# Optimization experiments

Hardware: AMD Instinct MI355X
Metric: run time of the kernel (lower is better)

Reference implementation:

```python
import math
import jax, jax.numpy as jnp
import numpy as np

QDEPTH = 8
WIDTH = 32
HEIGHT = 32
PIXELS = WIDTH * HEIGHT          # 1024
WIRES = int(math.ceil(math.log2(PIXELS)))  # 10, and PIXELS == 2**WIRES exactly
BATCH = 2048


def setup_inputs() -> dict:
    key = jax.random.key(0)
    k1, k2 = jax.random.split(key)
    x = jax.random.normal(k1, (BATCH, 1, WIDTH, HEIGHT), dtype=jnp.float32)
    # torch.randn(weight_shape) * 0.4
    weights = jax.random.normal(k2, (QDEPTH, WIRES, 3), dtype=jnp.float32) * 0.4
    return {"x": x, "weights": weights, "reps": 1}


def _apply_1q(s, U, wire):
    # s: (batch, 2, 2, ..., 2); apply 2x2 unitary U on qubit `wire` (axis wire+1)
    ax = wire + 1
    s = jnp.moveaxis(s, ax, -1)
    s = s @ U.T                      # new[..., i] = sum_j U[i, j] * old[..., j]
    return jnp.moveaxis(s, -1, ax)


def _apply_cnot(s, ctrl, tgt):
    # flip target bit on the control==1 half of the state
    c_ax = ctrl + 1
    t_ax = tgt + 1
    s0 = jnp.take(s, 0, axis=c_ax)
    s1 = jnp.take(s, 1, axis=c_ax)
    t = t_ax - 1 if t_ax > c_ax else t_ax
    s1 = jnp.flip(s1, axis=t)
    return jnp.stack([s0, s1], axis=c_ax)


def _rot_matrix(phi, theta, omega):
    # qml.Rot = RZ(phi) -> RY(theta) -> RZ(omega)
    c = jnp.cos(theta * 0.5)
    sn = jnp.sin(theta * 0.5)
    ep = jnp.exp(-0.5j * (phi + omega))   # e^{-i(phi+omega)/2}
    em = jnp.exp(-0.5j * (phi - omega))   # e^{-i(phi-omega)/2}
    return jnp.stack([
        jnp.stack([ep * c, -jnp.conj(em) * sn]),
        jnp.stack([em * sn, jnp.conj(ep) * c]),
    ]).astype(jnp.complex64)


def _circuit(psi, weights, reps):
    # psi: (batch, 2**WIRES) complex64 normalized state
    b = psi.shape[0]
    s = psi.reshape((b,) + (2,) * WIRES)
    w = jnp.tanh(weights)                 # qw_map.tanh
    # StronglyEntanglingLayers default ranges: r_l = l % (wires-1) + 1
    ranges = [(l % (WIRES - 1)) + 1 for l in range(QDEPTH)]
    for _ in range(reps):
        for l in range(QDEPTH):
            for q in range(WIRES):
                U = _rot_matrix(w[l, q, 0], w[l, q, 1], w[l, q, 2])
                s = _apply_1q(s, U, q)
            r = ranges[l]
            for q in range(WIRES):
                s = _apply_cnot(s, q, (q + r) % WIRES)
    return s.reshape(b, 2 ** WIRES)


def reference(x, weights, reps):
    b = x.shape[0]
    v = x.reshape(b, PIXELS)                       # b 1 w h -> b (w h)
    old_norm = jnp.linalg.norm(v, axis=-1, keepdims=True)
    psi = (v / old_norm).astype(jnp.complex64)     # real amplitudes, zero imag
    out = _circuit(psi, weights, reps)
    out = out * old_norm.astype(jnp.complex64)
    return out.reshape(b, 1, WIDTH, HEIGHT)
```

## Files before the change

### kernel.cpp

```cpp
#include <hip/hip_runtime.h>
#include <math.h>


#define WIRES   10
#define NSTATE  1024
#define QDEPTH  8
#define NBATCH  2048
#define NGATES  (QDEPTH * WIRES)

typedef float v2f __attribute__((ext_vector_type(2)));
typedef unsigned int v2u __attribute__((ext_vector_type(2)));
static __device__ __forceinline__ v2f s2(float x) { return (v2f){x, x}; }

__device__ __forceinline__ int perm_g(int j, int r) {
#pragma unroll
    for (int q = WIRES - 1; q >= 0; --q) {
        const int cb = 9 - q;
        const int tb = 9 - ((q + r) % WIRES);
        j ^= ((j >> cb) & 1) << tb;
    }
    return j;
}

template<int CTRL>
__device__ __forceinline__ float dppmov(float x) {
    return __int_as_float(__builtin_amdgcn_update_dpp(
        0, __float_as_int(x), CTRL, 0xF, 0xF, true));
}
#define FX1(v)  dppmov<0xB1>(v)
#define FX2(v)  dppmov<0x4E>(v)
#define FX4(v)  dppmov<0x1B>(dppmov<0x141>(v))
#define FX8(v)  dppmov<0x128>(v)

#if __has_builtin(__builtin_amdgcn_permlane16_swap)
static __device__ __forceinline__ float pl16swap(float x) {
    const v2u r = __builtin_amdgcn_permlane16_swap(
        __float_as_uint(x), __float_as_uint(x), false, false);
    return __uint_as_float((threadIdx.x & 16) ? r.x : r.y);
}
#define FX16(v) pl16swap(v)
#else
#define FX16(v) __shfl_xor((v), 16, 64)
#endif

#if __has_builtin(__builtin_amdgcn_permlane32_swap)
static __device__ __forceinline__ float pl32swap(float x) {
    const v2u r = __builtin_amdgcn_permlane32_swap(
        __float_as_uint(x), __float_as_uint(x), false, false);
    return __uint_as_float((threadIdx.x & 32) ? r.x : r.y);
}
#define FX32(v) pl32swap(v)
#else
#define FX32(v) __shfl_xor((v), 32, 64)
#endif

#define APPLY_LOCAL_PK(uptr, mask)                                            \
    {                                                                         \
        const float* __restrict__ u = (uptr);                                 \
        const float u00r=u[0], u00i=u[1], u01r=u[2], u01i=u[3];               \
        const float u10r=u[4], u10i=u[5], u11r=u[6], u11i=u[7];               \
        _Pragma("unroll")                                                     \
        for (int k0 = 0; k0 < 8; ++k0) {                                      \
            if (k0 & (mask)) continue;                                        \
            const int k1 = k0 | (mask);                                       \
            const v2f a0r = zr[k0], a0i = zi[k0];                             \
            const v2f a1r = zr[k1], a1i = zi[k1];                             \
            zr[k0] = s2(u00r)*a0r - s2(u00i)*a0i + s2(u01r)*a1r - s2(u01i)*a1i;\
            zi[k0] = s2(u00r)*a0i + s2(u00i)*a0r + s2(u01r)*a1i + s2(u01i)*a1r;\
            zr[k1] = s2(u10r)*a0r - s2(u10i)*a0i + s2(u11r)*a1r - s2(u11i)*a1i;\
            zi[k1] = s2(u10r)*a0i + s2(u10i)*a0r + s2(u11r)*a1i + s2(u11i)*a1r;\
        }                                                                     \
    }

#define LANE_GATE_PK(W, J, FETCH)                                             \
    {                                                                         \
        const float* __restrict__ u = gw + (W) * 8;                           \
        const bool hi = (lane >> (J)) & 1;                                    \
        const float c0r = hi ? u[6] : u[0], c0i = hi ? u[7] : u[1];           \
        const float c1r = hi ? u[4] : u[2], c1i = hi ? u[5] : u[3];           \
        _Pragma("unroll")                                                     \
        for (int k = 0; k < 8; ++k) {                                         \
            v2f pr, pi;                                                       \
            pr.x = FETCH(zr[k].x); pr.y = FETCH(zr[k].y);                     \
            pi.x = FETCH(zi[k].x); pi.y = FETCH(zi[k].y);                     \
            const v2f sr = zr[k], si = zi[k];                                 \
            zr[k] = s2(c0r)*sr - s2(c0i)*si + s2(c1r)*pr - s2(c1i)*pi;        \
            zi[k] = s2(c0r)*si + s2(c0i)*sr + s2(c1r)*pi + s2(c1i)*pr;        \
        }                                                                     \
    }

__global__ __launch_bounds__(64) void qsim_fused(
    const float* __restrict__ x,
    const float* __restrict__ weights,
    float* __restrict__ out,
    const int interleaved)
{
    __shared__ float lds[2 * NSTATE];
    __shared__ float cf[NGATES * 8];
    __shared__ int   gtl[QDEPTH * 16];
    __shared__ int   gaT[QDEPTH * 64];

    const int lane = threadIdx.x;
    const int b    = blockIdx.x;

    for (int g = lane; g < NGATES; g += 64) {
        const float phi   = tanhf(weights[g * 3 + 0]);
        const float theta = tanhf(weights[g * 3 + 1]);
        const float omega = tanhf(weights[g * 3 + 2]);
        const float c  = cosf(theta * 0.5f);
        const float sn = sinf(theta * 0.5f);
        const float a  = 0.5f * (phi + omega);
        const float bb = 0.5f * (phi - omega);
        const float ca = cosf(a),  sa = sinf(a);
        const float cb = cosf(bb), sb = sinf(bb);
        cf[g * 8 + 0] =  ca * c;  cf[g * 8 + 1] = -sa * c;
        cf[g * 8 + 2] = -cb * sn; cf[g * 8 + 3] = -sb * sn;
        cf[g * 8 + 4] =  cb * sn; cf[g * 8 + 5] = -sb * sn;
        cf[g * 8 + 6] =  ca * c;  cf[g * 8 + 7] =  sa * c;
    }
    for (int e = lane; e < QDEPTH * 16; e += 64) {
        const int l = e >> 4, t = e & 15;
        const int j = perm_g(t, l + 1);
        gtl[e] = ((j & 15) << 6) | (j >> 4);
    }
#pragma unroll
    for (int l = 0; l < QDEPTH; ++l) {
        const int j = perm_g(lane << 4, l + 1);
        gaT[l * 64 + lane] = ((j & 15) << 6) | (j >> 4);
    }

    v2f zr[8], zi[8];

    const float4* __restrict__ x4 =
        (const float4*)(x + ((size_t)b << 10) + (lane << 4));
    {
        const float4 v0 = x4[0], v1 = x4[1], v2 = x4[2], v3 = x4[3];
        zr[0].x=v0.x; zr[1].x=v0.y; zr[2].x=v0.z; zr[3].x=v0.w;
        zr[4].x=v1.x; zr[5].x=v1.y; zr[6].x=v1.z; zr[7].x=v1.w;
        zr[0].y=v2.x; zr[1].y=v2.y; zr[2].y=v2.z; zr[3].y=v2.w;
        zr[4].y=v3.x; zr[5].y=v3.y; zr[6].y=v3.z; zr[7].y=v3.w;
#pragma unroll
        for (int k = 0; k < 8; ++k) zi[k] = (v2f){0.f, 0.f};
    }

    for (int l = 0; l < QDEPTH; ++l) {
        const float* __restrict__ gw = cf + l * 80;

        APPLY_LOCAL_PK(gw + 9*8, 1)
        APPLY_LOCAL_PK(gw + 8*8, 2)
        APPLY_LOCAL_PK(gw + 7*8, 4)

        {
            const float* __restrict__ u = gw + 6*8;
            const v2f pAr = (v2f){u[0], u[6]};
            const v2f pAi = (v2f){u[1], u[7]};
            const v2f pBr = (v2f){u[2], u[4]};
            const v2f pBi = (v2f){u[3], u[5]};
#pragma unroll
            for (int k = 0; k < 8; ++k) {
                const v2f r  = zr[k], i = zi[k];
                const v2f rs = __builtin_shufflevector(r, r, 1, 0);
                const v2f is = __builtin_shufflevector(i, i, 1, 0);
                zr[k] = pAr*r - pAi*i + pBr*rs - pBi*is;
                zi[k] = pAr*i + pAi*r + pBr*is + pBi*rs;
            }
        }

        LANE_GATE_PK(5, 0, FX1)
        LANE_GATE_PK(4, 1, FX2)
        LANE_GATE_PK(3, 2, FX4)
        LANE_GATE_PK(2, 3, FX8)
        LANE_GATE_PK(1, 4, FX16)
        LANE_GATE_PK(0, 5, FX32)

#pragma unroll
        for (int k = 0; k < 8; ++k) {
            const int w = k * 64 + lane;
            lds[w]        = zr[k].x;
            lds[w + 512]  = zr[k].y;
            lds[w + 1024] = zi[k].x;
            lds[w + 1536] = zi[k].y;
        }
        const int ga = gaT[l * 64 + lane];
#pragma unroll
        for (int k = 0; k < 8; ++k) {
            const int a0 = ga ^ gtl[l * 16 + k];
            const int a1 = ga ^ gtl[l * 16 + k + 8];
            zr[k].x = lds[a0]; zi[k].x = lds[a0 + 1024];
            zr[k].y = lds[a1]; zi[k].y = lds[a1 + 1024];
        }
    }

    if (interleaved) {
        float2* __restrict__ o2 = (float2*)out;
        const size_t base = ((size_t)b << 10) + (lane << 4);
#pragma unroll
        for (int k = 0; k < 8; ++k) {
            o2[base + k]     = make_float2(zr[k].x, zi[k].x);
            o2[base + k + 8] = make_float2(zr[k].y, zi[k].y);
        }
    } else {
        float4* __restrict__ o4 = (float4*)(out + ((size_t)b << 10) + (lane << 4));
        o4[0] = make_float4(zr[0].x, zr[1].x, zr[2].x, zr[3].x);
        o4[1] = make_float4(zr[4].x, zr[5].x, zr[6].x, zr[7].x);
        o4[2] = make_float4(zr[0].y, zr[1].y, zr[2].y, zr[3].y);
        o4[3] = make_float4(zr[4].y, zr[5].y, zr[6].y, zr[7].y);
    }
}

extern "C" void kernel_launch(void* const* d_in, const int* in_sizes, int n_in,
                              void* d_out, int out_size, void* d_ws, size_t ws_size,
                              hipStream_t stream) {
    const float* x       = (const float*)d_in[0];
    const float* weights = (const float*)d_in[1];
    float* out = (float*)d_out;
    const int interleaved = (out_size >= 2 * NBATCH * NSTATE) ? 1 : 0;
    (void)d_ws; (void)ws_size;

    qsim_fused<<<NBATCH, 64, 0, stream>>>(x, weights, out, interleaved);
}
```

Measured before the change: 102.3 us.

## Keep gate coefficients in registers and broadcast them with readlane instead of LDS

Each lane now computes the coefficients of one or two gates into registers. Every gate's coefficients are fetched as wave-uniform scalars through readlane, so the per-gate LDS table reads are gone. The permutation XOR offsets are rebuilt from four readlane'd basis values per layer rather than loaded from a 16-entry LDS table. Together these aim to cut LDS traffic and latency inside the layer loop, at the cost of many readlane instructions (VALU to SGPR moves) and more register pressure from the coefficient arrays.

```diff
diff --git a/kernel.cpp b/kernel.cpp
--- a/kernel.cpp
+++ b/kernel.cpp
@@ -22,6 +22,19 @@
     return j;
 }
 
+#if __has_builtin(__builtin_amdgcn_readlane)
+static __device__ __forceinline__ int rli(int v, int idx) {
+    return __builtin_amdgcn_readlane(v, idx);
+}
+#else
+static __device__ __forceinline__ int rli(int v, int idx) {
+    return __shfl(v, idx, 64);
+}
+#endif
+static __device__ __forceinline__ float rlf(float v, int idx) {
+    return __int_as_float(rli(__float_as_int(v), idx));
+}
+
 template<int CTRL>
 __device__ __forceinline__ float dppmov(float x) {
     return __int_as_float(__builtin_amdgcn_update_dpp(
@@ -54,15 +67,33 @@
 #define FX32(v) __shfl_xor((v), 32, 64)
 #endif
 
-#define APPLY_LOCAL_PK(uptr, mask)                                            \
+__device__ __forceinline__ void gate_coeffs(
+    const float* __restrict__ w, int g, float (&c8)[8])
+{
+    const float phi   = tanhf(w[g * 3 + 0]);
+    const float theta = tanhf(w[g * 3 + 1]);
+    const float omega = tanhf(w[g * 3 + 2]);
+    const float c  = cosf(theta * 0.5f);
+    const float sn = sinf(theta * 0.5f);
+    const float a  = 0.5f * (phi + omega);
+    const float bb = 0.5f * (phi - omega);
+    const float ca = cosf(a),  sa = sinf(a);
+    const float cb = cosf(bb), sb = sinf(bb);
+    c8[0] =  ca * c;  c8[1] = -sa * c;
+    c8[2] = -cb * sn; c8[3] = -sb * sn;
+    c8[4] =  cb * sn; c8[5] = -sb * sn;
+    c8[6] =  ca * c;  c8[7] =  sa * c;
+}
+
+#define LOCAL_GATE(Q, MASK)                                                   \
     {                                                                         \
-        const float* __restrict__ u = (uptr);                                 \
-        const float u00r=u[0], u00i=u[1], u01r=u[2], u01i=u[3];               \
-        const float u10r=u[4], u10i=u[5], u11r=u[6], u11i=u[7];               \
+        const float u00r=getc(Q,0), u00i=getc(Q,1), u01r=getc(Q,2),           \
+                    u01i=getc(Q,3), u10r=getc(Q,4), u10i=getc(Q,5),           \
+                    u11r=getc(Q,6), u11i=getc(Q,7);                           \
         _Pragma("unroll")                                                     \
         for (int k0 = 0; k0 < 8; ++k0) {                                      \
-            if (k0 & (mask)) continue;                                        \
-            const int k1 = k0 | (mask);                                       \
+            if (k0 & (MASK)) continue;                                        \
+            const int k1 = k0 | (MASK);                                       \
             const v2f a0r = zr[k0], a0i = zi[k0];                             \
             const v2f a1r = zr[k1], a1i = zi[k1];                             \
             zr[k0] = s2(u00r)*a0r - s2(u00i)*a0i + s2(u01r)*a1r - s2(u01i)*a1i;\
@@ -72,12 +103,33 @@
         }                                                                     \
     }
 
-#define LANE_GATE_PK(W, J, FETCH)                                             \
+#define HSWAP_GATE(Q)                                                         \
     {                                                                         \
-        const float* __restrict__ u = gw + (W) * 8;                           \
+        const float u00r=getc(Q,0), u00i=getc(Q,1), u01r=getc(Q,2),           \
+                    u01i=getc(Q,3), u10r=getc(Q,4), u10i=getc(Q,5),           \
+                    u11r=getc(Q,6), u11i=getc(Q,7);                           \
+        const v2f pAr = (v2f){u00r, u11r};                                    \
+        const v2f pAi = (v2f){u00i, u11i};                                    \
+        const v2f pBr = (v2f){u01r, u10r};                                    \
+        const v2f pBi = (v2f){u01i, u10i};                                    \
+        _Pragma("unroll")                                                     \
+        for (int k = 0; k < 8; ++k) {                                         \
+            const v2f r  = zr[k], i = zi[k];                                  \
+            const v2f rs = __builtin_shufflevector(r, r, 1, 0);               \
+            const v2f is = __builtin_shufflevector(i, i, 1, 0);               \
+            zr[k] = pAr*r - pAi*i + pBr*rs - pBi*is;                          \
+            zi[k] = pAr*i + pAi*r + pBr*is + pBi*rs;                          \
+        }                                                                     \
+    }
+
+#define LANE_GATE(Q, J, FETCH)                                                \
+    {                                                                         \
+        const float u00r=getc(Q,0), u00i=getc(Q,1), u01r=getc(Q,2),           \
+                    u01i=getc(Q,3), u10r=getc(Q,4), u10i=getc(Q,5),           \
+                    u11r=getc(Q,6), u11i=getc(Q,7);                           \
         const bool hi = (lane >> (J)) & 1;                                    \
-        const float c0r = hi ? u[6] : u[0], c0i = hi ? u[7] : u[1];           \
-        const float c1r = hi ? u[4] : u[2], c1i = hi ? u[5] : u[3];           \
+        const float c0r = hi ? u11r : u00r, c0i = hi ? u11i : u00i;           \
+        const float c1r = hi ? u10r : u01r, c1i = hi ? u10i : u01i;           \
         _Pragma("unroll")                                                     \
         for (int k = 0; k < 8; ++k) {                                         \
             v2f pr, pi;                                                       \
@@ -89,39 +141,64 @@
         }                                                                     \
     }
 
-__global__ __launch_bounds__(64) void qsim_fused(
+template<typename GetC>
+__device__ __forceinline__ void layer_body(
+    v2f (&zr)[8], v2f (&zi)[8], GetC getc,
+    const int G0, const int G1, const int G2, const int G3,
+    const int ga, float* __restrict__ lds, const int lane)
+{
+    LOCAL_GATE(9, 1)
+    LOCAL_GATE(8, 2)
+    LOCAL_GATE(7, 4)
+    HSWAP_GATE(6)
+    LANE_GATE(5, 0, FX1)
+    LANE_GATE(4, 1, FX2)
+    LANE_GATE(3, 2, FX4)
+    LANE_GATE(2, 3, FX8)
+    LANE_GATE(1, 4, FX16)
+    LANE_GATE(0, 5, FX32)
+
+#pragma unroll
+    for (int k = 0; k < 8; ++k) {
+        const int w = k * 64 + lane;
+        lds[w]        = zr[k].x;
+        lds[w + 512]  = zr[k].y;
+        lds[w + 1024] = zi[k].x;
+        lds[w + 1536] = zi[k].y;
+    }
+    const int s01 = G0 ^ G1;
+    const int gkt[8] = {0, G0, G1, s01, G2, G2 ^ G0, G2 ^ G1, G2 ^ s01};
+#pragma unroll
+    for (int k = 0; k < 8; ++k) {
+        const int a0 = ga ^ gkt[k];
+        const int a1 = a0 ^ G3;
+        zr[k].x = lds[a0]; zi[k].x = lds[a0 + 1024];
+        zr[k].y = lds[a1]; zi[k].y = lds[a1 + 1024];
+    }
+}
+
+__global__ __launch_bounds__(64) void qsim_rl(
     const float* __restrict__ x,
     const float* __restrict__ weights,
     float* __restrict__ out,
     const int interleaved)
 {
     __shared__ float lds[2 * NSTATE];
-    __shared__ float cf[NGATES * 8];
-    __shared__ int   gtl[QDEPTH * 16];
     __shared__ int   gaT[QDEPTH * 64];
 
     const int lane = threadIdx.x;
     const int b    = blockIdx.x;
 
-    for (int g = lane; g < NGATES; g += 64) {
-        const float phi   = tanhf(weights[g * 3 + 0]);
-        const float theta = tanhf(weights[g * 3 + 1]);
-        const float omega = tanhf(weights[g * 3 + 2]);
-        const float c  = cosf(theta * 0.5f);
-        const float sn = sinf(theta * 0.5f);
-        const float a  = 0.5f * (phi + omega);
-        const float bb = 0.5f * (phi - omega);
-        const float ca = cosf(a),  sa = sinf(a);
-        const float cb = cosf(bb), sb = sinf(bb);
-        cf[g * 8 + 0] =  ca * c;  cf[g * 8 + 1] = -sa * c;
-        cf[g * 8 + 2] = -cb * sn; cf[g * 8 + 3] = -sb * sn;
-        cf[g * 8 + 4] =  cb * sn; cf[g * 8 + 5] = -sb * sn;
-        cf[g * 8 + 6] =  ca * c;  cf[g * 8 + 7] =  sa * c;
-    }
-    for (int e = lane; e < QDEPTH * 16; e += 64) {
-        const int l = e >> 4, t = e & 15;
-        const int j = perm_g(t, l + 1);
-        gtl[e] = ((j & 15) << 6) | (j >> 4);
+    float cA[8], cB[8];
+    gate_coeffs(weights, lane, cA);
+    gate_coeffs(weights, 64 + (lane & 15), cB);
+
+    int gv;
+    {
+        const int lg = (lane >> 2) & 7;
+        const int bb = lane & 3;
+        const int j  = perm_g(1 << bb, lg + 1);
+        gv = ((j & 15) << 6) | (j >> 4);
     }
 #pragma unroll
     for (int l = 0; l < QDEPTH; ++l) {
@@ -130,7 +207,6 @@
     }
 
     v2f zr[8], zi[8];
-
     const float4* __restrict__ x4 =
         (const float4*)(x + ((size_t)b << 10) + (lane << 4));
     {
@@ -143,52 +219,38 @@
         for (int k = 0; k < 8; ++k) zi[k] = (v2f){0.f, 0.f};
     }
 
-    for (int l = 0; l < QDEPTH; ++l) {
-        const float* __restrict__ gw = cf + l * 80;
-
-        APPLY_LOCAL_PK(gw + 9*8, 1)
-        APPLY_LOCAL_PK(gw + 8*8, 2)
-        APPLY_LOCAL_PK(gw + 7*8, 4)
-
-        {
-            const float* __restrict__ u = gw + 6*8;
-            const v2f pAr = (v2f){u[0], u[6]};
-            const v2f pAi = (v2f){u[1], u[7]};
-            const v2f pBr = (v2f){u[2], u[4]};
-            const v2f pBi = (v2f){u[3], u[5]};
-#pragma unroll
-            for (int k = 0; k < 8; ++k) {
-                const v2f r  = zr[k], i = zi[k];
-                const v2f rs = __builtin_shufflevector(r, r, 1, 0);
-                const v2f is = __builtin_shufflevector(i, i, 1, 0);
-                zr[k] = pAr*r - pAi*i + pBr*rs - pBi*is;
-                zi[k] = pAr*i + pAi*r + pBr*is + pBi*rs;
-            }
-        }
-
-        LANE_GATE_PK(5, 0, FX1)
-        LANE_GATE_PK(4, 1, FX2)
-        LANE_GATE_PK(3, 2, FX4)
-        LANE_GATE_PK(2, 3, FX8)
-        LANE_GATE_PK(1, 4, FX16)
-        LANE_GATE_PK(0, 5, FX32)
-
-#pragma unroll
-        for (int k = 0; k < 8; ++k) {
-            const int w = k * 64 + lane;
-            lds[w]        = zr[k].x;
-            lds[w + 512]  = zr[k].y;
-            lds[w + 1024] = zi[k].x;
-            lds[w + 1536] = zi[k].y;
-        }
-        const int ga = gaT[l * 64 + lane];
-#pragma unroll
-        for (int k = 0; k < 8; ++k) {
-            const int a0 = ga ^ gtl[l * 16 + k];
-            const int a1 = ga ^ gtl[l * 16 + k + 8];
-            zr[k].x = lds[a0]; zi[k].x = lds[a0 + 1024];
-            zr[k].y = lds[a1]; zi[k].y = lds[a1 + 1024];
-        }
+    int ga = gaT[lane];
+
+#pragma unroll 1
+    for (int l = 0; l < 6; ++l) {
+        const int sb = l * 10;
+        const int G0 = rli(gv, 4 * l + 0);
+        const int G1 = rli(gv, 4 * l + 1);
+        const int G2 = rli(gv, 4 * l + 2);
+        const int G3 = rli(gv, 4 * l + 3);
+        const int ga_nx = gaT[(l + 1) * 64 + lane];
+        layer_body(zr, zi,
+            [&](int q, int j) { return rlf(cA[j], sb + q); },
+            G0, G1, G2, G3, ga, lds, lane);
+        ga = ga_nx;
+    }
+    {
+        const int G0 = rli(gv, 24), G1 = rli(gv, 25);
+        const int G2 = rli(gv, 26), G3 = rli(gv, 27);
+        const int ga_nx = gaT[7 * 64 + lane];
+        layer_body(zr, zi,
+            [&](int q, int j) {
+                return (q < 4) ? rlf(cA[j], 60 + q) : rlf(cB[j], q - 4);
+            },
+            G0, G1, G2, G3, ga, lds, lane);
+        ga = ga_nx;
+    }
+    {
+        const int G0 = rli(gv, 28), G1 = rli(gv, 29);
+        const int G2 = rli(gv, 30), G3 = rli(gv, 31);
+        layer_body(zr, zi,
+            [&](int q, int j) { return rlf(cB[j], 6 + q); },
+            G0, G1, G2, G3, ga, lds, lane);
     }
 
     if (interleaved) {
@@ -217,5 +279,5 @@
     const int interleaved = (out_size >= 2 * NBATCH * NSTATE) ? 1 : 0;
     (void)d_ws; (void)ws_size;
 
-    qsim_fused<<<NBATCH, 64, 0, stream>>>(x, weights, out, interleaved);
-}
+    qsim_rl<<<NBATCH, 64, 0, stream>>>(x, weights, out, interleaved);
+}
```

Result: slower. 108.2 us (+5.7%).

## Track CNOT layers as lazy GF(2) basis changes instead of per-layer LDS permutes

Applied to the files above, without the earlier changes.

Replaces the per-layer LDS scatter/gather that implemented each CNOT ring with a compile-time GF(2) linear map tracking, so each rotation gate acts on a transformed bit mask with sign parity corrections, and only one final LDS permutation is done. Gate coefficients are computed in registers per lane and broadcast via readlane rather than staged through shared memory tables. This removes 7 LDS round trips and the shared-memory tables, at the cost of gates whose masks span multiple bits needing compound cross-lane xor shuffles and extra parity selects.

```diff
diff --git a/kernel.cpp b/kernel.cpp
--- a/kernel.cpp
+++ b/kernel.cpp
@@ -12,8 +12,7 @@
 typedef unsigned int v2u __attribute__((ext_vector_type(2)));
 static __device__ __forceinline__ v2f s2(float x) { return (v2f){x, x}; }
 
-__device__ __forceinline__ int perm_g(int j, int r) {
-#pragma unroll
+constexpr int perm_gc(int j, int r) {
     for (int q = WIRES - 1; q >= 0; --q) {
         const int cb = 9 - q;
         const int tb = 9 - ((q + r) % WIRES);
@@ -22,15 +21,65 @@
     return j;
 }
 
+struct QTab {
+    int m[QDEPTH][10];
+    int hi[QDEPTH][10];
+    int fin[10];
+};
+
+constexpr QTab build_qtab() {
+    QTab T{};
+    int m[10], fr[10];
+    for (int b = 0; b < 10; ++b) { m[b] = 1 << b; fr[b] = 1 << b; }
+    for (int l = 0; l < QDEPTH; ++l) {
+        for (int b = 0; b < 10; ++b) { T.m[l][b] = m[b]; T.hi[l][b] = fr[b]; }
+        const int r = (l % (WIRES - 1)) + 1;
+        int nm[10], nf[10];
+        for (int b = 0; b < 10; ++b) {
+            const int u = perm_gc(1 << b, r);
+            int acc = 0;
+            for (int c = 0; c < 10; ++c) if ((u >> c) & 1) acc ^= m[c];
+            nm[b] = acc;
+        }
+        int gi[10];
+        for (int b = 0; b < 10; ++b) gi[b] = 1 << b;
+        for (int q = 0; q <= 9; ++q) {
+            const int cb = 9 - q;
+            const int tb = 9 - ((q + r) % WIRES);
+            gi[tb] ^= gi[cb];
+        }
+        for (int b = 0; b < 10; ++b) {
+            int acc = 0;
+            for (int c = 0; c < 10; ++c) if ((gi[b] >> c) & 1) acc ^= fr[c];
+            nf[b] = acc;
+        }
+        for (int b = 0; b < 10; ++b) { m[b] = nm[b]; fr[b] = nf[b]; }
+    }
+    for (int b = 0; b < 10; ++b) T.fin[b] = m[b];
+    return T;
+}
+
+constexpr QTab QT = build_qtab();
+constexpr int word_map(int x) { return ((x & 15) << 6) | (x >> 4); }
+
+#if __has_builtin(__builtin_amdgcn_readlane)
+static __device__ __forceinline__ int rli(int v, int idx) {
+    return __builtin_amdgcn_readlane(v, idx);
+}
+#else
+static __device__ __forceinline__ int rli(int v, int idx) {
+    return __shfl(v, idx, 64);
+}
+#endif
+static __device__ __forceinline__ float rlf(float v, int idx) {
+    return __int_as_float(rli(__float_as_int(v), idx));
+}
+
 template<int CTRL>
 __device__ __forceinline__ float dppmov(float x) {
     return __int_as_float(__builtin_amdgcn_update_dpp(
         0, __float_as_int(x), CTRL, 0xF, 0xF, true));
 }
-#define FX1(v)  dppmov<0xB1>(v)
-#define FX2(v)  dppmov<0x4E>(v)
-#define FX4(v)  dppmov<0x1B>(dppmov<0x141>(v))
-#define FX8(v)  dppmov<0x128>(v)
 
 #if __has_builtin(__builtin_amdgcn_permlane16_swap)
 static __device__ __forceinline__ float pl16swap(float x) {
@@ -38,9 +87,10 @@
         __float_as_uint(x), __float_as_uint(x), false, false);
     return __uint_as_float((threadIdx.x & 16) ? r.x : r.y);
 }
-#define FX16(v) pl16swap(v)
 #else
-#define FX16(v) __shfl_xor((v), 16, 64)
+static __device__ __forceinline__ float pl16swap(float x) {
+    return __shfl_xor(x, 16, 64);
+}
 #endif
 
 #if __has_builtin(__builtin_amdgcn_permlane32_swap)
@@ -49,88 +99,144 @@
         __float_as_uint(x), __float_as_uint(x), false, false);
     return __uint_as_float((threadIdx.x & 32) ? r.x : r.y);
 }
-#define FX32(v) pl32swap(v)
 #else
-#define FX32(v) __shfl_xor((v), 32, 64)
+static __device__ __forceinline__ float pl32swap(float x) {
+    return __shfl_xor(x, 32, 64);
+}
 #endif
 
-#define APPLY_LOCAL_PK(uptr, mask)                                            \
+template<int ML>
+__device__ __forceinline__ float fxor(float x) {
+    float v = x;
+    constexpr int low = ML & 15;
+    if constexpr (low >= 4 && low <= 7)  v = dppmov<0x141>(v);
+    if constexpr (low >= 8 && low <= 11) v = dppmov<0x128>(v);
+    if constexpr (low >= 12)             v = dppmov<0x140>(v);
+    constexpr int q = (low < 4) ? low
+                    : (low < 8) ? (low ^ 7)
+                    : (low < 12) ? (low ^ 8) : (low ^ 15);
+    if constexpr (q == 1) v = dppmov<0xB1>(v);
+    if constexpr (q == 2) v = dppmov<0x4E>(v);
+    if constexpr (q == 3) v = dppmov<0x1B>(v);
+    if constexpr (ML & 16) v = pl16swap(v);
+    if constexpr (ML & 32) v = pl32swap(v);
+    return v;
+}
+
+template<int MH, int ML>
+__device__ __forceinline__ v2f fetch_pair(v2f v) {
+    v2f s;
+    if constexpr (MH) s = __builtin_shufflevector(v, v, 1, 0);
+    else              s = v;
+    if constexpr (ML != 0) { s.x = fxor<ML>(s.x); s.y = fxor<ML>(s.y); }
+    return s;
+}
+
+__device__ __forceinline__ void gate_coeffs4(
+    const float* __restrict__ w, int g, float (&c4)[4])
+{
+    const float phi   = tanhf(w[g * 3 + 0]);
+    const float theta = tanhf(w[g * 3 + 1]);
+    const float omega = tanhf(w[g * 3 + 2]);
+    const float c  = cosf(theta * 0.5f);
+    const float sn = sinf(theta * 0.5f);
+    const float a  = 0.5f * (phi + omega);
+    const float bb = 0.5f * (phi - omega);
+    const float ca = cosf(a),  sa = sinf(a);
+    const float cb = cosf(bb), sb = sinf(bb);
+    c4[0] =  ca * c;
+    c4[1] = -sa * c;
+    c4[2] = -cb * sn;
+    c4[3] = -sb * sn;
+}
+
+template<int M, int HI>
+__device__ __forceinline__ void gate_apply(
+    v2f (&zr)[8], v2f (&zi)[8],
+    const float u00r, const float u00i,
+    const float u01r, const float u01i, const int lane)
+{
+    constexpr int mk = M & 7;
+    constexpr int mh = (M >> 3) & 1;
+    constexpr int ml = M >> 4;
+    constexpr int hk = HI & 7;
+    constexpr int hh = (HI >> 3) & 1;
+    constexpr int hl = HI >> 4;
+
+    unsigned sL = 0u;
+    if constexpr (hl != 0)
+        sL = ((unsigned)(__popc(lane & hl) & 1)) << 31;
+
+    const float b0  = __uint_as_float(__float_as_uint(u00i) ^ sL);
+    const float b0n = __uint_as_float(__float_as_uint(b0) ^ 0x80000000u);
+    const float r0  = __uint_as_float(__float_as_uint(u01r) ^ sL);
+    const float r0n = __uint_as_float(__float_as_uint(r0) ^ 0x80000000u);
+    const v2f C0i0 = (v2f){b0,  hh ? b0n : b0};
+    const v2f C0i1 = (v2f){b0n, hh ? b0  : b0n};
+    const v2f C1r0 = (v2f){r0,  hh ? r0n : r0};
+    const v2f C1r1 = (v2f){r0n, hh ? r0  : r0n};
+    const v2f C0r  = s2(u00r);
+    const v2f C1i  = s2(u01i);
+
+#define QG_MATH(KK, PR, PI)                                                   \
     {                                                                         \
-        const float* __restrict__ u = (uptr);                                 \
-        const float u00r=u[0], u00i=u[1], u01r=u[2], u01i=u[3];               \
-        const float u10r=u[4], u10i=u[5], u11r=u[6], u11i=u[7];               \
-        _Pragma("unroll")                                                     \
-        for (int k0 = 0; k0 < 8; ++k0) {                                      \
-            if (k0 & (mask)) continue;                                        \
-            const int k1 = k0 | (mask);                                       \
-            const v2f a0r = zr[k0], a0i = zi[k0];                             \
-            const v2f a1r = zr[k1], a1i = zi[k1];                             \
-            zr[k0] = s2(u00r)*a0r - s2(u00i)*a0i + s2(u01r)*a1r - s2(u01i)*a1i;\
-            zi[k0] = s2(u00r)*a0i + s2(u00i)*a0r + s2(u01r)*a1i + s2(u01i)*a1r;\
-            zr[k1] = s2(u10r)*a0r - s2(u10i)*a0i + s2(u11r)*a1r - s2(u11i)*a1i;\
-            zi[k1] = s2(u10r)*a0i + s2(u10i)*a0r + s2(u11r)*a1i + s2(u11i)*a1r;\
-        }                                                                     \
-    }
-
-#define LANE_GATE_PK(W, J, FETCH)                                             \
-    {                                                                         \
-        const float* __restrict__ u = gw + (W) * 8;                           \
-        const bool hi = (lane >> (J)) & 1;                                    \
-        const float c0r = hi ? u[6] : u[0], c0i = hi ? u[7] : u[1];           \
-        const float c1r = hi ? u[4] : u[2], c1i = hi ? u[5] : u[3];           \
-        _Pragma("unroll")                                                     \
-        for (int k = 0; k < 8; ++k) {                                         \
-            v2f pr, pi;                                                       \
-            pr.x = FETCH(zr[k].x); pr.y = FETCH(zr[k].y);                     \
-            pi.x = FETCH(zi[k].x); pi.y = FETCH(zi[k].y);                     \
-            const v2f sr = zr[k], si = zi[k];                                 \
-            zr[k] = s2(c0r)*sr - s2(c0i)*si + s2(c1r)*pr - s2(c1i)*pi;        \
-            zi[k] = s2(c0r)*si + s2(c0i)*sr + s2(c1r)*pi + s2(c1i)*pr;        \
-        }                                                                     \
-    }
-
-__global__ __launch_bounds__(64) void qsim_fused(
+        const bool pc1 = (__popc((KK) & hk) & 1) != 0;                        \
+        const v2f C0i = pc1 ? C0i1 : C0i0;                                    \
+        const v2f C1r = pc1 ? C1r1 : C1r0;                                    \
+        const v2f sr = zr[(KK)], si = zi[(KK)];                               \
+        zr[(KK)] = C0r*sr - C0i*si + C1r*(PR) - C1i*(PI);                     \
+        zi[(KK)] = C0r*si + C0i*sr + C1r*(PI) + C1i*(PR);                     \
+    }
+
+    if constexpr (mk == 0) {
+#pragma unroll
+        for (int k = 0; k < 8; ++k) {
+            const v2f pr = fetch_pair<mh, ml>(zr[k]);
+            const v2f pi = fetch_pair<mh, ml>(zi[k]);
+            QG_MATH(k, pr, pi)
+        }
+    } else {
+#pragma unroll
+        for (int k0 = 0; k0 < 8; ++k0) {
+            if ((k0 ^ mk) < k0) continue;
+            const int k1 = k0 ^ mk;
+            const v2f p0r = fetch_pair<mh, ml>(zr[k1]);
+            const v2f p0i = fetch_pair<mh, ml>(zi[k1]);
+            const v2f p1r = fetch_pair<mh, ml>(zr[k0]);
+            const v2f p1i = fetch_pair<mh, ml>(zi[k0]);
+            QG_MATH(k0, p0r, p0i)
+            QG_MATH(k1, p1r, p1i)
+        }
+    }
+#undef QG_MATH
+}
+
+#define GA(L, B, G) gate_apply<QT.m[L][B], QT.hi[L][B]>(zr, zi,               \
+    rlf(cA[0], G), rlf(cA[1], G), rlf(cA[2], G), rlf(cA[3], G), lane);
+#define GB(L, B, G) gate_apply<QT.m[L][B], QT.hi[L][B]>(zr, zi,               \
+    rlf(cB[0], G), rlf(cB[1], G), rlf(cB[2], G), rlf(cB[3], G), lane);
+
+#define LAYER_A(L)                                                            \
+    GA(L, 0, (L)*10 + 9) GA(L, 1, (L)*10 + 8) GA(L, 2, (L)*10 + 7)            \
+    GA(L, 3, (L)*10 + 6) GA(L, 4, (L)*10 + 5) GA(L, 5, (L)*10 + 4)            \
+    GA(L, 6, (L)*10 + 3) GA(L, 7, (L)*10 + 2) GA(L, 8, (L)*10 + 1)            \
+    GA(L, 9, (L)*10 + 0)
+
+__global__ __launch_bounds__(64) void qsim_lazy(
     const float* __restrict__ x,
     const float* __restrict__ weights,
     float* __restrict__ out,
     const int interleaved)
 {
     __shared__ float lds[2 * NSTATE];
-    __shared__ float cf[NGATES * 8];
-    __shared__ int   gtl[QDEPTH * 16];
-    __shared__ int   gaT[QDEPTH * 64];
-
     const int lane = threadIdx.x;
     const int b    = blockIdx.x;
 
-    for (int g = lane; g < NGATES; g += 64) {
-        const float phi   = tanhf(weights[g * 3 + 0]);
-        const float theta = tanhf(weights[g * 3 + 1]);
-        const float omega = tanhf(weights[g * 3 + 2]);
-        const float c  = cosf(theta * 0.5f);
-        const float sn = sinf(theta * 0.5f);
-        const float a  = 0.5f * (phi + omega);
-        const float bb = 0.5f * (phi - omega);
-        const float ca = cosf(a),  sa = sinf(a);
-        const float cb = cosf(bb), sb = sinf(bb);
-        cf[g * 8 + 0] =  ca * c;  cf[g * 8 + 1] = -sa * c;
-        cf[g * 8 + 2] = -cb * sn; cf[g * 8 + 3] = -sb * sn;
-        cf[g * 8 + 4] =  cb * sn; cf[g * 8 + 5] = -sb * sn;
-        cf[g * 8 + 6] =  ca * c;  cf[g * 8 + 7] =  sa * c;
-    }
-    for (int e = lane; e < QDEPTH * 16; e += 64) {
-        const int l = e >> 4, t = e & 15;
-        const int j = perm_g(t, l + 1);
-        gtl[e] = ((j & 15) << 6) | (j >> 4);
-    }
-#pragma unroll
-    for (int l = 0; l < QDEPTH; ++l) {
-        const int j = perm_g(lane << 4, l + 1);
-        gaT[l * 64 + lane] = ((j & 15) << 6) | (j >> 4);
-    }
+    float cA[4], cB[4];
+    gate_coeffs4(weights, lane, cA);
+    gate_coeffs4(weights, 64 + (lane & 15), cB);
 
     v2f zr[8], zi[8];
-
     const float4* __restrict__ x4 =
         (const float4*)(x + ((size_t)b << 10) + (lane << 4));
     {
@@ -143,61 +249,42 @@
         for (int k = 0; k < 8; ++k) zi[k] = (v2f){0.f, 0.f};
     }
 
-    for (int l = 0; l < QDEPTH; ++l) {
-        const float* __restrict__ gw = cf + l * 80;
-
-        APPLY_LOCAL_PK(gw + 9*8, 1)
-        APPLY_LOCAL_PK(gw + 8*8, 2)
-        APPLY_LOCAL_PK(gw + 7*8, 4)
-
-        {
-            const float* __restrict__ u = gw + 6*8;
-            const v2f pAr = (v2f){u[0], u[6]};
-            const v2f pAi = (v2f){u[1], u[7]};
-            const v2f pBr = (v2f){u[2], u[4]};
-            const v2f pBi = (v2f){u[3], u[5]};
-#pragma unroll
-            for (int k = 0; k < 8; ++k) {
-                const v2f r  = zr[k], i = zi[k];
-                const v2f rs = __builtin_shufflevector(r, r, 1, 0);
-                const v2f is = __builtin_shufflevector(i, i, 1, 0);
-                zr[k] = pAr*r - pAi*i + pBr*rs - pBi*is;
-                zi[k] = pAr*i + pAi*r + pBr*is + pBi*rs;
-            }
-        }
-
-        LANE_GATE_PK(5, 0, FX1)
-        LANE_GATE_PK(4, 1, FX2)
-        LANE_GATE_PK(3, 2, FX4)
-        LANE_GATE_PK(2, 3, FX8)
-        LANE_GATE_PK(1, 4, FX16)
-        LANE_GATE_PK(0, 5, FX32)
-
-#pragma unroll
-        for (int k = 0; k < 8; ++k) {
-            const int w = k * 64 + lane;
-            lds[w]        = zr[k].x;
-            lds[w + 512]  = zr[k].y;
-            lds[w + 1024] = zi[k].x;
-            lds[w + 1536] = zi[k].y;
-        }
-        const int ga = gaT[l * 64 + lane];
-#pragma unroll
-        for (int k = 0; k < 8; ++k) {
-            const int a0 = ga ^ gtl[l * 16 + k];
-            const int a1 = ga ^ gtl[l * 16 + k + 8];
-            zr[k].x = lds[a0]; zi[k].x = lds[a0 + 1024];
-            zr[k].y = lds[a1]; zi[k].y = lds[a1 + 1024];
-        }
+    LAYER_A(0) LAYER_A(1) LAYER_A(2) LAYER_A(3) LAYER_A(4) LAYER_A(5)
+    GB(6, 0, 5) GB(6, 1, 4) GB(6, 2, 3) GB(6, 3, 2) GB(6, 4, 1) GB(6, 5, 0)
+    GA(6, 6, 63) GA(6, 7, 62) GA(6, 8, 61) GA(6, 9, 60)
+    GB(7, 0, 15) GB(7, 1, 14) GB(7, 2, 13) GB(7, 3, 12) GB(7, 4, 11)
+    GB(7, 5, 10) GB(7, 6,  9) GB(7, 7,  8) GB(7, 8,  7) GB(7, 9,  6)
+
+#pragma unroll
+    for (int k = 0; k < 8; ++k) {
+        const int w = k * 64 + lane;
+        lds[w]        = zr[k].x;
+        lds[w + 512]  = zr[k].y;
+        lds[w + 1024] = zi[k].x;
+        lds[w + 1536] = zi[k].y;
+    }
+    int base = 0;
+#pragma unroll
+    for (int j = 0; j < 6; ++j)
+        base ^= ((lane >> j) & 1) ? word_map(QT.fin[4 + j]) : 0;
+#pragma unroll
+    for (int k = 0; k < 8; ++k) {
+        const int at = ((k & 1) ? word_map(QT.fin[0]) : 0)
+                     ^ ((k & 2) ? word_map(QT.fin[1]) : 0)
+                     ^ ((k & 4) ? word_map(QT.fin[2]) : 0);
+        const int a0 = base ^ at;
+        const int a1 = a0 ^ word_map(QT.fin[3]);
+        zr[k].x = lds[a0]; zi[k].x = lds[a0 + 1024];
+        zr[k].y = lds[a1]; zi[k].y = lds[a1 + 1024];
     }
 
     if (interleaved) {
         float2* __restrict__ o2 = (float2*)out;
-        const size_t base = ((size_t)b << 10) + (lane << 4);
+        const size_t base2 = ((size_t)b << 10) + (lane << 4);
 #pragma unroll
         for (int k = 0; k < 8; ++k) {
-            o2[base + k]     = make_float2(zr[k].x, zi[k].x);
-            o2[base + k + 8] = make_float2(zr[k].y, zi[k].y);
+            o2[base2 + k]     = make_float2(zr[k].x, zi[k].x);
+            o2[base2 + k + 8] = make_float2(zr[k].y, zi[k].y);
         }
     } else {
         float4* __restrict__ o4 = (float4*)(out + ((size_t)b << 10) + (lane << 4));
@@ -217,5 +304,5 @@
     const int interleaved = (out_size >= 2 * NBATCH * NSTATE) ? 1 : 0;
     (void)d_ws; (void)ws_size;
 
-    qsim_fused<<<NBATCH, 64, 0, stream>>>(x, weights, out, interleaved);
-}
+    qsim_lazy<<<NBATCH, 64, 0, stream>>>(x, weights, out, interleaved);
+}
```

New measurement: 250.6 us. +144.9%, slower.
